# Optimization experiments

Measured on AMD Instinct MI355X. Metric: run time of the kernel, lower is better.

Reference implementation:

```python
import jax, jax.numpy as jnp
import numpy as np

N = 50000       # nodes
E = 800000      # directed edges (src -> dst)
INDIM, HID, OUT = 256, 128, 64
NEG_SLOPE = 0.2  # PyG GATConv default negative_slope


def gat_layer(x, src, dst, W, a_src, a_dst, b, n_nodes):
    """Single-head PyG-style GATConv with self-loops already in (src, dst)."""
    h = x @ W.T                                   # [N, F_out]
    alpha_src = h @ a_src                         # [N]
    alpha_dst = h @ a_dst                         # [N]
    # per-edge attention logits, LeakyReLU
    e = jax.nn.leaky_relu(alpha_src[src] + alpha_dst[dst], NEG_SLOPE)  # [E']
    # segment softmax grouped by destination node (numerically stable)
    m = jnp.full((n_nodes,), -jnp.inf, e.dtype).at[dst].max(e)
    ee = jnp.exp(e - m[dst])
    denom = jax.ops.segment_sum(ee, dst, num_segments=n_nodes)
    alpha = ee / denom[dst]                       # [E']
    # weighted scatter-add of source messages
    out = jax.ops.segment_sum(h[src] * alpha[:, None], dst, num_segments=n_nodes)
    return out + b


def setup_inputs() -> dict:
    key = jax.random.key(0)
    ks = jax.random.split(key, 10)
    s = 0.1
    return {
        "x": jax.random.normal(ks[0], (N, INDIM), jnp.float32),
        "edge_index": jax.random.randint(ks[1], (2, E), 0, N, dtype=jnp.int32),
        "W1": jax.random.normal(ks[2], (HID, INDIM), jnp.float32) * s,
        "a_src1": jax.random.normal(ks[3], (HID,), jnp.float32) * s,
        "a_dst1": jax.random.normal(ks[4], (HID,), jnp.float32) * s,
        "b1": jnp.zeros((HID,), jnp.float32),
        "W2": jax.random.normal(ks[5], (OUT, HID), jnp.float32) * s,
        "a_src2": jax.random.normal(ks[6], (OUT,), jnp.float32) * s,
        "a_dst2": jax.random.normal(ks[7], (OUT,), jnp.float32) * s,
        "b2": jnp.zeros((OUT,), jnp.float32),
    }


def reference(x, edge_index, W1, a_src1, a_dst1, b1, W2, a_src2, a_dst2, b2):
    n_nodes = x.shape[0]
    # PyG GATConv default add_self_loops=True
    loops = jnp.arange(n_nodes, dtype=edge_index.dtype)
    src = jnp.concatenate([edge_index[0], loops])
    dst = jnp.concatenate([edge_index[1], loops])
    h = gat_layer(x, src, dst, W1, a_src1, a_dst1, b1, n_nodes)
    h = jax.nn.relu(h)
    h = gat_layer(h, src, dst, W2, a_src2, a_dst2, b2, n_nodes)
    return h
```

## Files before the change

### kernel.cpp

```cpp
#include <hip/hip_runtime.h>
#include <hip/hip_bf16.h>
#include <math.h>

#define NN 50000
#define EE 800000
#define INDIM 256
#define HID 128
#define OUTF 64
#define NEG_SLOPE 0.2f
#define CAP 64

typedef __attribute__((ext_vector_type(8))) short bf16x8;
typedef __attribute__((ext_vector_type(4))) float f32x4;

__device__ inline float bflo(unsigned p) { return __uint_as_float(p << 16); }
__device__ inline float bfhi(unsigned p) { return __uint_as_float(p & 0xffff0000u); }
__device__ inline unsigned f2bf(float f) {
    unsigned u = __float_as_uint(f);
    return (u + 0x7fffu + ((u >> 16) & 1u)) >> 16;
}
__device__ inline float leaky(float l) { return (l > 0.f) ? l : NEG_SLOPE * l; }

template <typename AT, int BN, int WR, int WC, bool FA, bool FAL>
__device__ inline void gemm_body(const AT* __restrict__ A,
                                 const float* __restrict__ B,
                                 unsigned short* __restrict__ Cb,
                                 const float* __restrict__ a_s,
                                 const float* __restrict__ a_d,
                                 float* __restrict__ asrc,
                                 float* __restrict__ adst,
                                 int N, int K, int bid)
{
    constexpr int BM = 128, LD = 40;
    constexpr int MF = (BM / WR) / 16;
    constexpr int NF = (BN / WC) / 16;
    static_assert(!FA || WC == 1, "register alpha needs full cols per wave");
    __shared__ unsigned short As[BM * LD];
    __shared__ unsigned short Bs[BN * LD];
    __shared__ float al_s[FAL ? 2 * BM : 2];

    const int tid = threadIdx.x;
    const int wave = tid >> 6, lane = tid & 63;
    const int wr = wave / WC, wc = wave % WC;
    const int wrow0 = wr * (BM / WR);
    const int wcol0 = wc * (BN / WC);
    const int row0 = bid * BM;
    const int lrow = lane & 15, lkg = lane >> 4;

    if constexpr (FAL) {
        for (int i = tid; i < 2 * BM; i += 256) al_s[i] = 0.f;
    }

    f32x4 acc[MF][NF];
    #pragma unroll
    for (int mi = 0; mi < MF; ++mi)
        #pragma unroll
        for (int ni = 0; ni < NF; ++ni) acc[mi][ni] = 0.f;

    for (int k0 = 0; k0 < K; k0 += 32) {
        if constexpr (sizeof(AT) == 4) {
            #pragma unroll
            for (int i = tid; i < BM * 8; i += 256) {
                int row = i >> 3, kq = i & 7;
                float4 v = make_float4(0.f, 0.f, 0.f, 0.f);
                int gr = row0 + row;
                if (gr < N) v = *(const float4*)((const float*)A + (size_t)gr * K + k0 + kq * 4);
                unsigned p0 = f2bf(v.x) | (f2bf(v.y) << 16);
                unsigned p1 = f2bf(v.z) | (f2bf(v.w) << 16);
                *(uint2*)&As[row * LD + kq * 4] = make_uint2(p0, p1);
            }
        } else {
            #pragma unroll
            for (int i = tid; i < BM * 4; i += 256) {
                int row = i >> 2, q = i & 3;
                uint4 v = make_uint4(0u, 0u, 0u, 0u);
                int gr = row0 + row;
                if (gr < N) v = *(const uint4*)((const unsigned short*)A + (size_t)gr * K + k0 + q * 8);
                *(uint4*)&As[row * LD + q * 8] = v;
            }
        }
        #pragma unroll
        for (int i = tid; i < BN * 8; i += 256) {
            int row = i >> 3, kq = i & 7;
            float4 v = *(const float4*)(B + (size_t)row * K + k0 + kq * 4);
            unsigned p0 = f2bf(v.x) | (f2bf(v.y) << 16);
            unsigned p1 = f2bf(v.z) | (f2bf(v.w) << 16);
            *(uint2*)&Bs[row * LD + kq * 4] = make_uint2(p0, p1);
        }
        __syncthreads();

        bf16x8 af[MF], bfr[NF];
        #pragma unroll
        for (int mi = 0; mi < MF; ++mi)
            af[mi] = *(const bf16x8*)&As[(wrow0 + mi * 16 + lrow) * LD + lkg * 8];
        #pragma unroll
        for (int ni = 0; ni < NF; ++ni)
            bfr[ni] = *(const bf16x8*)&Bs[(wcol0 + ni * 16 + lrow) * LD + lkg * 8];
        #pragma unroll
        for (int mi = 0; mi < MF; ++mi)
            #pragma unroll
            for (int ni = 0; ni < NF; ++ni)
                acc[mi][ni] = __builtin_amdgcn_mfma_f32_16x16x32_bf16(
                    af[mi], bfr[ni], acc[mi][ni], 0, 0, 0);
        __syncthreads();
    }

    if constexpr (FA || FAL) {
        float asv[NF], adv[NF];
        #pragma unroll
        for (int ni = 0; ni < NF; ++ni) {
            int c = wcol0 + ni * 16 + lrow;
            asv[ni] = a_s[c]; adv[ni] = a_d[c];
        }
        #pragma unroll
        for (int mi = 0; mi < MF; ++mi)
            #pragma unroll
            for (int r = 0; r < 4; ++r) {
                float ps = 0.f, pd = 0.f;
                #pragma unroll
                for (int ni = 0; ni < NF; ++ni) {
                    ps = fmaf(acc[mi][ni][r], asv[ni], ps);
                    pd = fmaf(acc[mi][ni][r], adv[ni], pd);
                }
                #pragma unroll
                for (int d = 1; d < 16; d <<= 1) {
                    ps += __shfl_xor(ps, d);
                    pd += __shfl_xor(pd, d);
                }
                int lr_ = wrow0 + mi * 16 + lkg * 4 + r;
                if constexpr (FA) {
                    int gr = row0 + lr_;
                    if (lrow == 0 && gr < N) { asrc[gr] = ps; adst[gr] = pd; }
                } else {
                    if (lrow == 0) {
                        atomicAdd(&al_s[lr_], ps);
                        atomicAdd(&al_s[BM + lr_], pd);
                    }
                }
            }
    }

    #pragma unroll
    for (int mi = 0; mi < MF; ++mi)
        #pragma unroll
        for (int ni = 0; ni < NF; ++ni)
            #pragma unroll
            for (int r = 0; r < 4; ++r) {
                int gr = row0 + wrow0 + mi * 16 + lkg * 4 + r;
                int gc = wcol0 + ni * 16 + lrow;
                if (gr < N)
                    Cb[(size_t)gr * BN + gc] = (unsigned short)f2bf(acc[mi][ni][r]);
            }

    if constexpr (FAL) {
        __syncthreads();
        if (tid < BM) {
            int gr = row0 + tid;
            if (gr < N) { asrc[gr] = al_s[tid]; adst[gr] = al_s[BM + tid]; }
        }
    }
}

__global__ __launch_bounds__(256) void fused_gemm1_scatter(
    const float* __restrict__ x, const float* __restrict__ W1,
    unsigned short* __restrict__ h1b,
    const float* __restrict__ a_s, const float* __restrict__ a_d,
    float* __restrict__ asrc, float* __restrict__ adst,
    const int* __restrict__ src_in, const int* __restrict__ dst_in,
    int* __restrict__ cnt, unsigned short* __restrict__ csr,
    int N, int K, int GB, int E)
{
    if ((int)blockIdx.x < GB) {
        gemm_body<float, 128, 2, 2, false, true>(x, W1, h1b, a_s, a_d,
                                                 asrc, adst, N, K, blockIdx.x);
    } else {
        int e = (blockIdx.x - GB) * 256 + threadIdx.x;
        int tot = E + N;
        if (e >= tot) return;
        int d, s;
        if (e < E) { d = dst_in[e]; s = src_in[e]; }
        else       { d = e - E;    s = d; }
        int r = atomicAdd(&cnt[d], 1);
        if (r < CAP) csr[((size_t)d << 6) + r] = (unsigned short)s;
    }
}

__global__ __launch_bounds__(256) void gemm2_alpha_kernel(
    const unsigned short* __restrict__ A, const float* __restrict__ B,
    unsigned short* __restrict__ Cb,
    const float* __restrict__ a_s, const float* __restrict__ a_d,
    float* __restrict__ asrc, float* __restrict__ adst, int N, int K)
{
    gemm_body<unsigned short, 64, 4, 1, true, false>(A, B, Cb, a_s, a_d,
                                                     asrc, adst, N, K, blockIdx.x);
}

template <int F, bool RELU, bool OUTBF>
__global__ __launch_bounds__(256) void aggregate_kernel(
    const unsigned short* __restrict__ hb, const unsigned short* __restrict__ csr,
    const int* __restrict__ cnt_arr, const float* __restrict__ asrc,
    const float* __restrict__ adst, const float* __restrict__ bias,
    void* __restrict__ outv, int n)
{
    constexpr int G = F / 8;
    constexpr int EPI = 64 / G;
    constexpr int STEP = EPI * 4;
    int wave = (int)((blockIdx.x * (size_t)blockDim.x + threadIdx.x) >> 6);
    int lane = threadIdx.x & 63;
    if (wave >= n) return;
    const size_t beg = (size_t)wave << 6;
    int cntv = cnt_arr[wave];
    cntv = (cntv > CAP) ? CAP : cntv;
    const float ad = adst[wave];
    const int grp = lane / G, fl = lane % G;

    float acc[8];
    #pragma unroll
    for (int p = 0; p < 8; ++p) acc[p] = 0.f;

    int s = 0;
    float e = 0.f;
    if (lane < cntv) { s = (int)csr[beg + lane]; e = __expf(leaky(asrc[s] + ad)); }
    float denom = e;
    #pragma unroll
    for (int d = 32; d > 0; d >>= 1) denom += __shfl_xor(denom, d);
    float w = e * __fdividef(1.f, denom);

    for (int jj0 = 0; jj0 < cntv; jj0 += STEP) {
        uint4 q[4];
        float wj[4];
        #pragma unroll
        for (int u = 0; u < 4; ++u) {
            int sel = jj0 + u * EPI + grp;
            int sj = __shfl(s, sel);
            wj[u] = __shfl(w, sel);
            q[u] = make_uint4(0u, 0u, 0u, 0u);
            if (sel < cntv)
                q[u] = *(const uint4*)(hb + (size_t)sj * F + fl * 8);
        }
        #pragma unroll
        for (int u = 0; u < 4; ++u) {
            acc[0] += wj[u] * bflo(q[u].x); acc[1] += wj[u] * bfhi(q[u].x);
            acc[2] += wj[u] * bflo(q[u].y); acc[3] += wj[u] * bfhi(q[u].y);
            acc[4] += wj[u] * bflo(q[u].z); acc[5] += wj[u] * bfhi(q[u].z);
            acc[6] += wj[u] * bflo(q[u].w); acc[7] += wj[u] * bfhi(q[u].w);
        }
    }

    #pragma unroll
    for (int d = G; d < 64; d <<= 1)
        #pragma unroll
        for (int p = 0; p < 8; ++p) acc[p] += __shfl_xor(acc[p], d);

    if (lane < G) {
        float v[8];
        #pragma unroll
        for (int p = 0; p < 8; ++p) {
            v[p] = acc[p] + bias[fl * 8 + p];
            if (RELU) v[p] = fmaxf(v[p], 0.f);
        }
        if constexpr (OUTBF) {
            unsigned short* o = (unsigned short*)outv + (size_t)wave * F + fl * 8;
            uint4 pk;
            pk.x = f2bf(v[0]) | (f2bf(v[1]) << 16);
            pk.y = f2bf(v[2]) | (f2bf(v[3]) << 16);
            pk.z = f2bf(v[4]) | (f2bf(v[5]) << 16);
            pk.w = f2bf(v[6]) | (f2bf(v[7]) << 16);
            *(uint4*)o = pk;
        } else {
            float* o = (float*)outv + (size_t)wave * F + fl * 8;
            *(float4*)o       = make_float4(v[0], v[1], v[2], v[3]);
            *(float4*)(o + 4) = make_float4(v[4], v[5], v[6], v[7]);
        }
    }
}

extern "C" void kernel_launch(void* const* d_in, const int* in_sizes, int n_in,
                              void* d_out, int out_size, void* d_ws, size_t ws_size,
                              hipStream_t stream)
{
    const float* x      = (const float*)d_in[0];
    const int*   ei     = (const int*)d_in[1];
    const float* W1     = (const float*)d_in[2];
    const float* a_src1 = (const float*)d_in[3];
    const float* a_dst1 = (const float*)d_in[4];
    const float* b1     = (const float*)d_in[5];
    const float* W2     = (const float*)d_in[6];
    const float* a_src2 = (const float*)d_in[7];
    const float* a_dst2 = (const float*)d_in[8];
    const float* b2     = (const float*)d_in[9];
    float* out = (float*)d_out;

    const int N = NN, E = EE;
    const int* src_in = ei;
    const int* dst_in = ei + E;

    char* p = (char*)d_ws;
    unsigned short* h1b   = (unsigned short*)p; p += (size_t)N * HID * 2;
    unsigned short* hmidb = (unsigned short*)p; p += (size_t)N * HID * 2;
    unsigned short* h2b   = (unsigned short*)p; p += (size_t)N * OUTF * 2;
    float* asrc = (float*)p; p += (size_t)N * 4;
    float* adst = (float*)p; p += (size_t)N * 4;
    int* cnt    = (int*)p;   p += (size_t)N * 4;
    unsigned short* csr = (unsigned short*)p; p += (size_t)N * CAP * 2;

    hipMemsetAsync(cnt, 0, (size_t)N * 4, stream);

    const int GB = (N + 127) / 128;
    const int SB = (E + N + 255) / 256;
    const int nwb = (N * 64 + 255) / 256;

    fused_gemm1_scatter<<<GB + SB, 256, 0, stream>>>(
        x, W1, h1b, a_src1, a_dst1, asrc, adst, src_in, dst_in, cnt, csr,
        N, INDIM, GB, E);
    aggregate_kernel<HID, true, true><<<nwb, 256, 0, stream>>>(
        h1b, csr, cnt, asrc, adst, b1, hmidb, N);

    gemm2_alpha_kernel<<<GB, 256, 0, stream>>>(hmidb, W2, h2b, a_src2, a_dst2,
                                               asrc, adst, N, HID);
    aggregate_kernel<OUTF, false, false><<<nwb, 256, 0, stream>>>(
        h2b, csr, cnt, asrc, adst, b2, out, N);

    (void)in_sizes; (void)n_in; (void)out_size; (void)ws_size;
}
```

Baseline: 233.3 us.

## Replace global-atomic CSR scatter with two-pass bucketed binning in shared memory

Swaps the per-edge global atomicAdd scatter into the capped CSR for a two-pass scheme. Edges are first binned into 256-node buckets using shared-memory histograms and scans, with one global atomic per bucket per block. A second kernel then builds each bucket's CSR rows in LDS and writes them out with coalesced stores. The goal is to cut contended, uncoalesced global atomics and scattered 2-byte writes, at the cost of an extra kernel launch, an intermediate bucket buffer reused from h2b, and a fixed bucket capacity (BCAP) that could drop edges on skewed graphs.

```diff
diff --git a/kernel.cpp b/kernel.cpp
--- a/kernel.cpp
+++ b/kernel.cpp
@@ -9,6 +9,11 @@
 #define OUTF 64
 #define NEG_SLOPE 0.2f
 #define CAP 64
+
+#define NB ((NN + 255) >> 8)
+#define BCAP 6144
+#define CHUNK 2048
+#define EPT 8
 
 typedef __attribute__((ext_vector_type(8))) short bf16x8;
 typedef __attribute__((ext_vector_type(4))) float f32x4;
@@ -161,28 +166,124 @@
     }
 }
 
-__global__ __launch_bounds__(256) void fused_gemm1_scatter(
+__device__ inline void bin_body(int bb,
+                                const int* __restrict__ src_in,
+                                const int* __restrict__ dst_in,
+                                unsigned* __restrict__ gbucket,
+                                int* __restrict__ bcnt,
+                                int E, int tot)
+{
+    __shared__ int h_hist[256];
+    __shared__ int h_scan[256];
+    __shared__ int h_ofs[256];
+    __shared__ int h_gbase[256];
+    __shared__ unsigned grp[CHUNK];
+
+    const int tid = threadIdx.x;
+    const int e0 = bb * CHUNK;
+    const int cntc = min(CHUNK, tot - e0);
+
+    h_hist[tid] = 0;
+    __syncthreads();
+
+    unsigned pk[EPT];
+    bool val[EPT];
+    #pragma unroll
+    for (int u = 0; u < EPT; ++u) {
+        int e = e0 + u * 256 + tid;
+        val[u] = (e < tot);
+        if (val[u]) {
+            int d, s;
+            if (e < E) { d = dst_in[e]; s = src_in[e]; }
+            else       { d = e - E;    s = d; }
+            pk[u] = ((unsigned)d << 16) | (unsigned)s;
+            atomicAdd(&h_hist[d >> 8], 1);
+        }
+    }
+    __syncthreads();
+
+    int v = h_hist[tid];
+    int incl = v;
+    h_scan[tid] = incl;
+    __syncthreads();
+    for (int off = 1; off < 256; off <<= 1) {
+        int t = (tid >= off) ? h_scan[tid - off] : 0;
+        __syncthreads();
+        incl += t;
+        h_scan[tid] = incl;
+        __syncthreads();
+    }
+    int excl = incl - v;
+    h_scan[tid] = excl;
+    h_ofs[tid] = excl;
+    h_gbase[tid] = (tid < NB && v > 0) ? atomicAdd(&bcnt[tid], v) : 0;
+    __syncthreads();
+
+    #pragma unroll
+    for (int u = 0; u < EPT; ++u)
+        if (val[u]) {
+            int b = pk[u] >> 24;
+            int pos = atomicAdd(&h_ofs[b], 1);
+            grp[pos] = pk[u];
+        }
+    __syncthreads();
+
+    for (int i = tid; i < cntc; i += 256) {
+        unsigned p = grp[i];
+        int b = p >> 24;
+        int gp = h_gbase[b] + (i - h_scan[b]);
+        if (gp < BCAP) gbucket[(size_t)b * BCAP + gp] = p;
+    }
+}
+
+__global__ __launch_bounds__(256) void fused_gemm1_bin(
     const float* __restrict__ x, const float* __restrict__ W1,
     unsigned short* __restrict__ h1b,
     const float* __restrict__ a_s, const float* __restrict__ a_d,
     float* __restrict__ asrc, float* __restrict__ adst,
     const int* __restrict__ src_in, const int* __restrict__ dst_in,
-    int* __restrict__ cnt, unsigned short* __restrict__ csr,
+    unsigned* __restrict__ gbucket, int* __restrict__ bcnt,
     int N, int K, int GB, int E)
 {
     if ((int)blockIdx.x < GB) {
         gemm_body<float, 128, 2, 2, false, true>(x, W1, h1b, a_s, a_d,
                                                  asrc, adst, N, K, blockIdx.x);
     } else {
-        int e = (blockIdx.x - GB) * 256 + threadIdx.x;
-        int tot = E + N;
-        if (e >= tot) return;
-        int d, s;
-        if (e < E) { d = dst_in[e]; s = src_in[e]; }
-        else       { d = e - E;    s = d; }
-        int r = atomicAdd(&cnt[d], 1);
-        if (r < CAP) csr[((size_t)d << 6) + r] = (unsigned short)s;
-    }
+        bin_body(blockIdx.x - GB, src_in, dst_in, gbucket, bcnt, E, E + N);
+    }
+}
+
+__global__ __launch_bounds__(256) void csr_build(
+    const unsigned* __restrict__ gbucket, const int* __restrict__ bcnt,
+    int* __restrict__ cnt, unsigned short* __restrict__ csr, int N)
+{
+    __shared__ int c2[256];
+    __shared__ unsigned short cl[256 * CAP];
+
+    const int b = blockIdx.x;
+    const int tid = threadIdx.x;
+    c2[tid] = 0;
+    __syncthreads();
+
+    int len = bcnt[b];
+    if (len > BCAP) len = BCAP;
+    for (int i = tid; i < len; i += 256) {
+        unsigned p = gbucket[(size_t)b * BCAP + i];
+        int dl = (p >> 16) & 255;
+        int s  = p & 0xffff;
+        int r = atomicAdd(&c2[dl], 1);
+        if (r < CAP) cl[(dl << 6) + r] = (unsigned short)s;
+    }
+    __syncthreads();
+
+    int d = (b << 8) + tid;
+    if (d < N) cnt[d] = c2[tid];
+
+    int rows = N - (b << 8);
+    rows = (rows > 256) ? 256 : rows;
+    const uint4* sp = (const uint4*)cl;
+    uint4* dp = (uint4*)(csr + (((size_t)b << 8) << 6));
+    for (int i = tid; i < rows * 8; i += 256) dp[i] = sp[i];
 }
 
 __global__ __launch_bounds__(256) void gemm2_alpha_kernel(
@@ -303,16 +404,20 @@
     float* adst = (float*)p; p += (size_t)N * 4;
     int* cnt    = (int*)p;   p += (size_t)N * 4;
     unsigned short* csr = (unsigned short*)p; p += (size_t)N * CAP * 2;
-
-    hipMemsetAsync(cnt, 0, (size_t)N * 4, stream);
-
-    const int GB = (N + 127) / 128;
-    const int SB = (E + N + 255) / 256;
-    const int nwb = (N * 64 + 255) / 256;
-
-    fused_gemm1_scatter<<<GB + SB, 256, 0, stream>>>(
-        x, W1, h1b, a_src1, a_dst1, asrc, adst, src_in, dst_in, cnt, csr,
-        N, INDIM, GB, E);
+    int* bcnt = (int*)p; p += 256 * 4;
+    unsigned* gbucket = (unsigned*)h2b;
+
+    hipMemsetAsync(bcnt, 0, 256 * 4, stream);
+
+    const int GB   = (N + 127) / 128;
+    const int BINB = (E + N + CHUNK - 1) / CHUNK;
+    const int nwb  = (N * 64 + 255) / 256;
+
+    fused_gemm1_bin<<<GB + BINB, 256, 0, stream>>>(
+        x, W1, h1b, a_src1, a_dst1, asrc, adst, src_in, dst_in,
+        gbucket, bcnt, N, INDIM, GB, E);
+    csr_build<<<NB, 256, 0, stream>>>(gbucket, bcnt, cnt, csr, N);
+
     aggregate_kernel<HID, true, true><<<nwb, 256, 0, stream>>>(
         h1b, csr, cnt, asrc, adst, b1, hmidb, N);
 
```

After: 221.7 us. 5.0% less time.
